# Performance work log

Hardware: AMD Instinct MI355X
Metric: run time of the kernel (lower is better)

## Reference

```python
import jax, jax.numpy as jnp
import numpy as np

N, C, E = 50000, 128, 10
INV3 = float(1.0 / np.sqrt(3.0))
NORM_C = float(1.0 / np.sqrt(C))


def setup_inputs() -> dict:
    key = jax.random.key(0)
    ks = jax.random.split(key, 14)
    node_feats = jax.random.normal(ks[0], (N, 4 * C), jnp.float32)
    elem = jax.random.randint(ks[1], (N,), 0, E)
    node_attrs = jax.nn.one_hot(elem, E, dtype=jnp.float32)
    sc = jax.random.normal(ks[2], (N, 4 * C), jnp.float32)
    tp2_w = jax.random.normal(ks[3], (4, C), jnp.float32)
    tp3_w = jax.random.normal(ks[4], (8, C), jnp.float32)
    coef0_w0 = jax.random.normal(ks[5], (E, C, C), jnp.float32)
    coef0_w1 = jax.random.normal(ks[6], (E, C, C), jnp.float32)
    coef1_w0 = jax.random.normal(ks[7], (E, 2 * C, C), jnp.float32)
    coef1_w1 = jax.random.normal(ks[8], (E, 2 * C, C), jnp.float32)
    coef2_w0 = jax.random.normal(ks[9], (E, 4 * C, C), jnp.float32)
    coef2_w1 = jax.random.normal(ks[10], (E, 4 * C, C), jnp.float32)
    lin_w0 = jax.random.normal(ks[11], (C, C), jnp.float32)
    lin_w1 = jax.random.normal(ks[12], (C, C), jnp.float32)
    return dict(node_feats=node_feats, node_attrs=node_attrs, sc=sc,
                tp2_w=tp2_w, tp3_w=tp3_w,
                coef0_w0=coef0_w0, coef0_w1=coef0_w1,
                coef1_w0=coef1_w0, coef1_w1=coef1_w1,
                coef2_w0=coef2_w0, coef2_w1=coef2_w1,
                lin_w0=lin_w0, lin_w1=lin_w1)


def acc_elem_linear(x0, x1, attrs, W0, W1):
    # per-element linear combine: one-hot attrs select element-specific weights
    norm = 1.0 / np.sqrt(x0.shape[1])
    o0 = jnp.zeros((attrs.shape[0], W0.shape[2]), x0.dtype)
    o1 = jnp.zeros((attrs.shape[0], W1.shape[2], 3), x1.dtype)
    for e in range(W0.shape[0]):  # small fixed element count
        a = attrs[:, e]
        o0 = o0 + a[:, None] * (x0 @ W0[e])
        o1 = o1 + a[:, None, None] * jnp.einsum('ncm,cd->ndm', x1, W1[e])
    return o0 * norm, o1 * norm


def reference(node_feats, node_attrs, sc, tp2_w, tp3_w,
              coef0_w0, coef0_w1, coef1_w0, coef1_w1,
              coef2_w0, coef2_w1, lin_w0, lin_w1):
    n = node_feats.shape[0]
    s = node_feats[:, :C]                      # [N,C]    0e
    v = node_feats[:, C:].reshape(n, C, 3)     # [N,C,3]  1o

    # nu=2: channelwise (uuu) CG tensor product, paths filtered to {0e,1o}
    m0a = tp2_w[0] * s * s                                # 0e x 0e -> 0e
    m1a = tp2_w[1][:, None] * s[:, :, None] * v * INV3    # 0e x 1o -> 1o
    m1b = tp2_w[2][:, None] * v * s[:, :, None] * INV3    # 1o x 0e -> 1o
    m0b = tp2_w[3] * jnp.sum(v * v, axis=-1) * INV3       # 1o x 1o -> 0e

    # nu=3: mid (A0=m0a 0e, A1=m1a 1o, A2=m1b 1o, A3=m0b 0e) x node_feats
    q0 = jnp.concatenate([
        tp3_w[0] * m0a * s,
        tp3_w[3] * jnp.sum(m1a * v, -1) * INV3,
        tp3_w[5] * jnp.sum(m1b * v, -1) * INV3,
        tp3_w[6] * m0b * s], axis=1)                      # [N,4C]
    q1 = jnp.concatenate([
        tp3_w[1][:, None] * m0a[:, :, None] * v * INV3,
        tp3_w[2][:, None] * m1a * s[:, :, None] * INV3,
        tp3_w[4][:, None] * m1b * s[:, :, None] * INV3,
        tp3_w[7][:, None] * m0b[:, :, None] * v * INV3], axis=1)  # [N,4C,3]

    f0, f1 = acc_elem_linear(s, v, node_attrs, coef0_w0, coef0_w1)
    g0, g1 = acc_elem_linear(jnp.concatenate([m0a, m0b], 1),
                             jnp.concatenate([m1a, m1b], 1),
                             node_attrs, coef1_w0, coef1_w1)
    h0, h1 = acc_elem_linear(q0, q1, node_attrs, coef2_w0, coef2_w1)
    o0 = f0 + g0 + h0
    o1 = f1 + g1 + h1

    o0 = (o0 @ lin_w0) * NORM_C
    o1 = jnp.einsum('ncm,cd->ndm', o1, lin_w1) * NORM_C
    out = jnp.concatenate([o0, o1.reshape(n, -1)], axis=1) + sc
    return out
```

## Files before the change

kernel.cpp:

```cpp
#include <hip/hip_runtime.h>

typedef unsigned short u16;
typedef __attribute__((ext_vector_type(8))) short short8;
typedef __attribute__((ext_vector_type(4))) float f32x4;

#define N_NODES 50000
#define C_ 128
#define E_ 10
#define NT_ 16
#define NBLK_MAIN 3200
#define NBLK_S 196
#define K0_ 640
#define K1_ 512

#define WF0_BYTES (E_ * 8 * 20 * 512 * 2)
#define WF1_BYTES (E_ * 8 * 16 * 512 * 2)
#define CNT_OFF    (WF0_BYTES + WF1_BYTES)
#define BLKCNT_OFF (CNT_OFF + 64)
#define BASE_OFF   (BLKCNT_OFF + 8192)
#define LIST_OFF   (BASE_OFF + 8192)

__device__ __forceinline__ u16 f2bf(float f){ union{unsigned u; float f;} v; v.f = f; unsigned u = v.u; u += 0x7FFFu + ((u>>16)&1u); return (u16)(u>>16); }
__device__ __forceinline__ unsigned cvtpk(float a, float b){
    unsigned r;
    asm("v_cvt_pk_bf16_f32 %0, %1, %2" : "=v"(r) : "v"(a), "v"(b));
    return r;
}

__global__ __launch_bounds__(256) void prep_weights_kernel(
    const float* __restrict__ tp2, const float* __restrict__ tp3,
    const float* __restrict__ c00, const float* __restrict__ c10, const float* __restrict__ c20,
    const float* __restrict__ c01, const float* __restrict__ c11, const float* __restrict__ c21,
    const float* __restrict__ lin0, const float* __restrict__ lin1,
    u16* __restrict__ WF0, u16* __restrict__ WF1)
{
    const int b = blockIdx.x;
    const int e = b / 9, kb = b % 9;
    const int which = (kb >= 5) ? 1 : 0;
    const int seg = which ? kb - 5 : kb;
    const float* __restrict__ lin = which ? lin1 : lin0;

    __shared__ u16 R[128 * 136];
    __shared__ u16 LT[128 * 132];

    const int tid = threadIdx.x;
    const float NC = 0.08838834764831845f;

    for (int t = tid; t < 128 * 32; t += 256) {
        const int jj = t >> 5, c4 = (t & 31) << 2;
        const float4 v = *(const float4*)(lin + jj * 128 + c4);
        LT[(c4 + 0) * 132 + jj] = f2bf(v.x * NC);
        LT[(c4 + 1) * 132 + jj] = f2bf(v.y * NC);
        LT[(c4 + 2) * 132 + jj] = f2bf(v.z * NC);
        LT[(c4 + 3) * 132 + jj] = f2bf(v.w * NC);
    }

    {
        const int c = tid >> 1, jh = (tid & 1) * 64;
        const float i128 = 0.08838834764831845f;
        const float i256 = 0.0625f;
        const float i512 = 0.04419417382415922f;
        const float I3   = 0.5773502691896258f;
        const float I9   = I3 * I3;
        const float t2_0 = tp2[0*C_+c], t2_1 = tp2[1*C_+c], t2_2 = tp2[2*C_+c], t2_3 = tp2[3*C_+c];
        const float t3_0 = tp3[0*C_+c], t3_1 = tp3[1*C_+c], t3_2 = tp3[2*C_+c];
        const float t3_3 = tp3[3*C_+c], t3_4 = tp3[4*C_+c], t3_5 = tp3[5*C_+c];
        const float t3_6 = tp3[6*C_+c], t3_7 = tp3[7*C_+c];

        const float* P0; const float* P1 = nullptr; const float* P2 = nullptr;
        float a0 = 0.f, a1 = 0.f, a2 = 0.f;
        if (!which) {
            const float* C0 = c00 + (size_t)e * C_   * C_;
            const float* C1 = c10 + (size_t)e * 2*C_ * C_;
            const float* C2 = c20 + (size_t)e * 4*C_ * C_;
            switch (seg) {
            case 0: P0 = C0 + c*C_;          a0 = i128; break;
            case 1: P0 = C1 + c*C_;          a0 = t2_0 * i256; break;
            case 2: P0 = C1 + (C_+c)*C_;     a0 = t2_3 * I3 * i256; break;
            case 3: P0 = C2 + c*C_;          a0 = t3_0 * t2_0 * i512; break;
            default:
                P0 = C2 + (C_+c)*C_;         a0 = t3_3 * t2_1 * I9 * i512;
                P1 = C2 + (2*C_+c)*C_;       a1 = t3_5 * t2_2 * I9 * i512;
                P2 = C2 + (3*C_+c)*C_;       a2 = t3_6 * t2_3 * I3 * i512; break;
            }
        } else {
            const float* C0 = c01 + (size_t)e * C_   * C_;
            const float* C1 = c11 + (size_t)e * 2*C_ * C_;
            const float* C2 = c21 + (size_t)e * 4*C_ * C_;
            switch (seg) {
            case 0: P0 = C0 + c*C_;          a0 = i128; break;
            case 1: P0 = C1 + c*C_;          a0 = t2_1 * I3 * i256;
                    P1 = C1 + (C_+c)*C_;     a1 = t2_2 * I3 * i256; break;
            case 2: P0 = C2 + c*C_;          a0 = t3_1 * t2_0 * I3 * i512;
                    P1 = C2 + (C_+c)*C_;     a1 = t3_2 * t2_1 * I9 * i512;
                    P2 = C2 + (2*C_+c)*C_;   a2 = t3_4 * t2_2 * I9 * i512; break;
            default: P0 = C2 + (3*C_+c)*C_;  a0 = t3_7 * t2_3 * I9 * i512; break;
            }
        }
        for (int j4 = 0; j4 < 64; j4 += 4) {
            const int jj = jh + j4;
            const float4 v = *(const float4*)(P0 + jj);
            float r0 = a0*v.x, r1 = a0*v.y, r2 = a0*v.z, r3 = a0*v.w;
            if (P1) {
                const float4 u = *(const float4*)(P1 + jj);
                r0 += a1*u.x; r1 += a1*u.y; r2 += a1*u.z; r3 += a1*u.w;
            }
            if (P2) {
                const float4 u = *(const float4*)(P2 + jj);
                r0 += a2*u.x; r1 += a2*u.y; r2 += a2*u.z; r3 += a2*u.w;
            }
            ushort4 st; st.x = f2bf(r0); st.y = f2bf(r1); st.z = f2bf(r2); st.w = f2bf(r3);
            *(ushort4*)&R[c * 136 + jj] = st;
        }
    }
    __syncthreads();

    const int wv = tid >> 6, l = tid & 63;
    const int lcol = l & 15, gD = l >> 4;
    f32x4 acc[2][8];
#pragma unroll
    for (int s = 0; s < 2; ++s)
#pragma unroll
        for (int t = 0; t < 8; ++t) acc[s][t] = (f32x4){0.f, 0.f, 0.f, 0.f};

#pragma unroll
    for (int ks2 = 0; ks2 < 4; ++ks2) {
        const int jj0 = ks2 * 32 + gD * 4;
        short8 bf[8];
#pragma unroll
        for (int t = 0; t < 8; ++t) {
            const int colB = t * 16 + lcol;
            union { unsigned long long q[2]; short8 v; } u;
            u.q[0] = *(const unsigned long long*)&LT[colB * 132 + jj0];
            u.q[1] = *(const unsigned long long*)&LT[colB * 132 + jj0 + 16];
            bf[t] = u.v;
        }
#pragma unroll
        for (int s = 0; s < 2; ++s) {
            const int krow = (wv + s * 4) * 16 + lcol;
            union { unsigned long long q[2]; short8 v; } ua;
            ua.q[0] = *(const unsigned long long*)&R[krow * 136 + jj0];
            ua.q[1] = *(const unsigned long long*)&R[krow * 136 + jj0 + 16];
#pragma unroll
            for (int t = 0; t < 8; ++t)
                acc[s][t] = __builtin_amdgcn_mfma_f32_16x16x32_bf16(ua.v, bf[t], acc[s][t], 0, 0, 0);
        }
    }

#pragma unroll
    for (int s = 0; s < 2; ++s) {
#pragma unroll
        for (int r = 0; r < 4; ++r) {
            const int k = (wv + s * 4) * 16 + 4 * gD + r;
            const int ks = k >> 5, r2 = k & 31;
            const int eh = r2 >> 4, g2 = (r2 >> 2) & 3, el = r2 & 3;
            const int elem = eh * 4 + el;
            const int lanef = lcol + 16 * g2;
            const int slot = seg * 4 + ks;
#pragma unroll
            for (int t = 0; t < 8; ++t) {
                const u16 wvl = f2bf(acc[s][t][r]);
                if (!which) WF0[(((size_t)(e*8 + t))*20 + slot)*512 + lanef*8 + elem] = wvl;
                else        WF1[(((size_t)(e*8 + t))*16 + slot)*512 + lanef*8 + elem] = wvl;
            }
        }
    }
}

__global__ void count_kernel(const float* __restrict__ attrs, int* __restrict__ blkcnt) {
    __shared__ int lcnt[E_];
    const int blk = blockIdx.x, tid = threadIdx.x;
    if (tid < E_) lcnt[tid] = 0;
    __syncthreads();
    const int n = blk * 256 + tid;
    if (n < N_NODES) {
        const float* a = attrs + (size_t)n * E_;
        int e = 0;
#pragma unroll
        for (int i = 0; i < E_; ++i) if (a[i] > 0.5f) e = i;
        atomicAdd(&lcnt[e], 1);
    }
    __syncthreads();
    if (tid < E_) blkcnt[tid * 200 + blk] = lcnt[tid];
}

__global__ void scan_kernel(const int* __restrict__ blkcnt, int* __restrict__ base,
                            int* __restrict__ cnt) {
    const int e = threadIdx.x;
    if (e < E_) {
        int acc = 0;
        for (int b = 0; b < NBLK_S; ++b) { base[e * 200 + b] = acc; acc += blkcnt[e * 200 + b]; }
        cnt[e] = acc;
    }
}

__global__ void scatter_kernel(const float* __restrict__ attrs, const int* __restrict__ base,
                               int* __restrict__ lists) {
    __shared__ int wcnt[4][E_];
    __shared__ int wbase[4][E_];
    const int blk = blockIdx.x, tid = threadIdx.x;
    const int wv = tid >> 6, lane = tid & 63;
    const int n = blk * 256 + tid;
    int e = -1;
    if (n < N_NODES) {
        e = 0;
        const float* a = attrs + (size_t)n * E_;
#pragma unroll
        for (int i = 0; i < E_; ++i) if (a[i] > 0.5f) e = i;
    }
    int rank = 0;
#pragma unroll
    for (int v = 0; v < E_; ++v) {
        const unsigned long long m = __ballot(e == v);
        if (e == v) rank = __popcll(m & ((1ull << lane) - 1ull));
        if (lane == 0) wcnt[wv][v] = __popcll(m);
    }
    __syncthreads();
    if (tid < E_) {
        int acc = 0;
#pragma unroll
        for (int w2 = 0; w2 < 4; ++w2) { wbase[w2][tid] = acc; acc += wcnt[w2][tid]; }
    }
    __syncthreads();
    if (n < N_NODES) lists[e * N_NODES + base[e * 200 + blk] + wbase[wv][e] + rank] = n;
}

__global__ __launch_bounds__(256, 3) void main_kernel(
    const float* __restrict__ feats, const float* __restrict__ sc,
    const int* __restrict__ cnt, const int* __restrict__ lists,
    const u16* __restrict__ WF0, const u16* __restrict__ WF1,
    float* __restrict__ out)
{
    __shared__ __align__(16) u16 A2[2][24 * 512];

    const int tid = threadIdx.x;
    const int bxr = blockIdx.x;
    const int bx = (bxr & 7) * (NBLK_MAIN / 8) + (bxr >> 3);

    int e = -1, tile = 0, accT = 0;
#pragma unroll
    for (int i = 0; i < E_; ++i) {
        const int ci = cnt[i];
        const int t = (ci + NT_ - 1) >> 4;
        if (e < 0 && bx < accT + t) { e = i; tile = bx - accT; }
        accT += t;
    }
    if (e < 0) return;
    const int nvalid = min(NT_, cnt[e] - tile * NT_);

    const int node = tid >> 4;
    const int cg   = tid & 15;
    const int n = (node < nvalid) ? lists[e*N_NODES + tile*NT_ + node] : -1;

    float4 s0 = make_float4(0.f,0.f,0.f,0.f), s1 = s0;
    float4 v4[6];
#pragma unroll
    for (int k = 0; k < 6; ++k) v4[k] = s0;
    if (n >= 0) {
        const float* f = feats + (size_t)n * 512;
        s0 = *(const float4*)(f + cg*8);
        s1 = *(const float4*)(f + cg*8 + 4);
#pragma unroll
        for (int k = 0; k < 6; ++k) v4[k] = *(const float4*)(f + 128 + cg*24 + 4*k);
    }
    float S[8]  = {s0.x,s0.y,s0.z,s0.w, s1.x,s1.y,s1.z,s1.w};
    float V[24] = {v4[0].x,v4[0].y,v4[0].z,v4[0].w, v4[1].x,v4[1].y,v4[1].z,v4[1].w,
                   v4[2].x,v4[2].y,v4[2].z,v4[2].w, v4[3].x,v4[3].y,v4[3].z,v4[3].w,
                   v4[4].x,v4[4].y,v4[4].z,v4[4].w, v4[5].x,v4[5].y,v4[5].z,v4[5].w};
    float S2[8], VV[8];
#pragma unroll
    for (int i = 0; i < 8; ++i) {
        S2[i] = S[i]*S[i];
        VV[i] = V[3*i]*V[3*i] + V[3*i+1]*V[3*i+1] + V[3*i+2]*V[3*i+2];
    }

    const int ksl   = cg >> 2;
    const int eh    = (cg >> 1) & 1;
    const int gb    = (cg & 1) * 2;
    const int lp0   = (node + 16*gb)        ^ (ksl << 1);
    const int lp1   = (node + 16*(gb + 1))  ^ (ksl << 1);
    const int off0  = lp0*8 + 4*eh;
    const int off1  = lp1*8 + 4*eh;

#define WSLOT(BUF, SLOT, V0,V1,V2,V3,V4,V5,V6,V7) do { \
        uint2 w0_, w1_; \
        w0_.x = cvtpk((V0),(V1)); w0_.y = cvtpk((V2),(V3)); \
        w1_.x = cvtpk((V4),(V5)); w1_.y = cvtpk((V6),(V7)); \
        *(uint2*)&A2[BUF][(SLOT)*512 + off0] = w0_; \
        *(uint2*)&A2[BUF][(SLOT)*512 + off1] = w1_; \
    } while (0)

    WSLOT(0, 0*4 + ksl, S[0],S[1],S[2],S[3],S[4],S[5],S[6],S[7]);
    WSLOT(0, 1*4 + ksl, S2[0],S2[1],S2[2],S2[3],S2[4],S2[5],S2[6],S2[7]);
    WSLOT(0, 2*4 + ksl, VV[0],VV[1],VV[2],VV[3],VV[4],VV[5],VV[6],VV[7]);
    WSLOT(0, 3*4 + ksl, S2[0]*S[0],S2[1]*S[1],S2[2]*S[2],S2[3]*S[3],
                        S2[4]*S[4],S2[5]*S[5],S2[6]*S[6],S2[7]*S[7]);
    WSLOT(0, 4*4 + ksl, S[0]*VV[0],S[1]*VV[1],S[2]*VV[2],S[3]*VV[3],
                        S[4]*VV[4],S[5]*VV[5],S[6]*VV[6],S[7]*VV[7]);
    __syncthreads();

    const int w4 = tid >> 6, l = tid & 63;
    const int lcol = l & 15, g = l >> 4;
    const int col0 = (2*w4)*16 + lcol;
    const int col1 = col0 + 16;
    const u16* WB0a = WF0 + ((size_t)(e*8 + 2*w4))     * (20*512) + l*8;
    const u16* WB0b = WB0a + 20*512;
    const u16* WB1a = WF1 + ((size_t)(e*8 + 2*w4))     * (16*512) + l*8;
    const u16* WB1b = WB1a + 16*512;

    f32x4 accS0 = {0.f,0.f,0.f,0.f}, accS1 = accS0;
    f32x4 accV[3][2];
#pragma unroll
    for (int m = 0; m < 3; ++m) { accV[m][0] = accS0; accV[m][1] = accS0; }

#pragma unroll
    for (int m = 0; m < 3; ++m) {
        WSLOT(1, m*4 + ksl,     V[0*3+m],V[1*3+m],V[2*3+m],V[3*3+m],
                                V[4*3+m],V[5*3+m],V[6*3+m],V[7*3+m]);
        WSLOT(1, (3+m)*4 + ksl, S[0]*V[0*3+m],S[1]*V[1*3+m],S[2]*V[2*3+m],S[3]*V[3*3+m],
                                S[4]*V[4*3+m],S[5]*V[5*3+m],S[6]*V[6*3+m],S[7]*V[7*3+m]);
    }
#pragma unroll
    for (int ks2 = 0; ks2 < 4; ++ks2) {
        const int lp8 = (l ^ (ks2 << 1)) * 8;
#pragma unroll
        for (int p = 0; p < 5; ++p) {
            const short8 a  = *(const short8*)&A2[0][(p*4 + ks2)*512 + lp8];
            const short8 b0 = *(const short8*)(WB0a + (p*4 + ks2)*512);
            const short8 b1 = *(const short8*)(WB0b + (p*4 + ks2)*512);
            accS0 = __builtin_amdgcn_mfma_f32_16x16x32_bf16(a, b0, accS0, 0, 0, 0);
            accS1 = __builtin_amdgcn_mfma_f32_16x16x32_bf16(a, b1, accS1, 0, 0, 0);
        }
    }
    __syncthreads();

#pragma unroll
    for (int m = 0; m < 3; ++m) {
        WSLOT(0, m*4 + ksl,     S2[0]*V[0*3+m],S2[1]*V[1*3+m],S2[2]*V[2*3+m],S2[3]*V[3*3+m],
                                S2[4]*V[4*3+m],S2[5]*V[5*3+m],S2[6]*V[6*3+m],S2[7]*V[7*3+m]);
        WSLOT(0, (3+m)*4 + ksl, VV[0]*V[0*3+m],VV[1]*V[1*3+m],VV[2]*V[2*3+m],VV[3]*V[3*3+m],
                                VV[4]*V[4*3+m],VV[5]*V[5*3+m],VV[6]*V[6*3+m],VV[7]*V[7*3+m]);
    }
    float4 scR[8];
#pragma unroll
    for (int j = 0; j < 8; ++j) scR[j] = make_float4(0.f,0.f,0.f,0.f);
    if (n >= 0) {
        const float* sp = sc + (size_t)n * 512 + cg * 4;
#pragma unroll
        for (int j = 0; j < 8; ++j) scR[j] = *(const float4*)(sp + 64*j);
    }
#pragma unroll
    for (int ks2 = 0; ks2 < 4; ++ks2) {
        const int lp8 = (l ^ (ks2 << 1)) * 8;
#pragma unroll
        for (int q = 0; q < 2; ++q) {
            const short8 b0 = *(const short8*)(WB1a + (q*4 + ks2)*512);
            const short8 b1 = *(const short8*)(WB1b + (q*4 + ks2)*512);
#pragma unroll
            for (int m = 0; m < 3; ++m) {
                const short8 a = *(const short8*)&A2[1][((q*3 + m)*4 + ks2)*512 + lp8];
                accV[m][0] = __builtin_amdgcn_mfma_f32_16x16x32_bf16(a, b0, accV[m][0], 0, 0, 0);
                accV[m][1] = __builtin_amdgcn_mfma_f32_16x16x32_bf16(a, b1, accV[m][1], 0, 0, 0);
            }
        }
    }
    __syncthreads();

#pragma unroll
    for (int ks2 = 0; ks2 < 4; ++ks2) {
        const int lp8 = (l ^ (ks2 << 1)) * 8;
#pragma unroll
        for (int q = 0; q < 2; ++q) {
            const short8 b0 = *(const short8*)(WB1a + ((2+q)*4 + ks2)*512);
            const short8 b1 = *(const short8*)(WB1b + ((2+q)*4 + ks2)*512);
#pragma unroll
            for (int m = 0; m < 3; ++m) {
                const short8 a = *(const short8*)&A2[0][((q*3 + m)*4 + ks2)*512 + lp8];
                accV[m][0] = __builtin_amdgcn_mfma_f32_16x16x32_bf16(a, b0, accV[m][0], 0, 0, 0);
                accV[m][1] = __builtin_amdgcn_mfma_f32_16x16x32_bf16(a, b1, accV[m][1], 0, 0, 0);
            }
        }
    }
    __syncthreads();

    float* OutB = (float*)&A2[0][0];
#pragma unroll
    for (int r = 0; r < 4; ++r) {
        const int nd = 4*g + r;
        OutB[nd*516 + col0] = accS0[r];
        OutB[nd*516 + col1] = accS1[r];
#pragma unroll
        for (int m = 0; m < 3; ++m) {
            OutB[nd*516 + 128 + 3*col0 + m] = accV[m][0][r];
            OutB[nd*516 + 128 + 3*col1 + m] = accV[m][1][r];
        }
    }
    __syncthreads();

    if (n >= 0) {
        const size_t gb2 = (size_t)n * 512 + cg * 4;
#pragma unroll
        for (int j = 0; j < 8; ++j) {
            const float4 vres = *(const float4*)&OutB[node*516 + cg*4 + 64*j];
            float4 o;
            o.x = vres.x + scR[j].x; o.y = vres.y + scR[j].y;
            o.z = vres.z + scR[j].z; o.w = vres.w + scR[j].w;
            *(float4*)(out + gb2 + 64*j) = o;
        }
    }
#undef WSLOT
}

extern "C" void kernel_launch(void* const* d_in, const int* in_sizes, int n_in,
                              void* d_out, int out_size, void* d_ws, size_t ws_size,
                              hipStream_t stream) {
    const float* feats = (const float*)d_in[0];
    const float* attrs = (const float*)d_in[1];
    const float* sc    = (const float*)d_in[2];
    const float* tp2   = (const float*)d_in[3];
    const float* tp3   = (const float*)d_in[4];
    const float* c00   = (const float*)d_in[5];
    const float* c01   = (const float*)d_in[6];
    const float* c10   = (const float*)d_in[7];
    const float* c11   = (const float*)d_in[8];
    const float* c20   = (const float*)d_in[9];
    const float* c21   = (const float*)d_in[10];
    const float* lin0  = (const float*)d_in[11];
    const float* lin1  = (const float*)d_in[12];
    float* out = (float*)d_out;

    char* ws = (char*)d_ws;
    u16* WF0    = (u16*)(ws);
    u16* WF1    = (u16*)(ws + WF0_BYTES);
    int* cnt    = (int*)(ws + CNT_OFF);
    int* blkcnt = (int*)(ws + BLKCNT_OFF);
    int* base   = (int*)(ws + BASE_OFF);
    int* lists  = (int*)(ws + LIST_OFF);

    hipLaunchKernelGGL(prep_weights_kernel, dim3(E_*9), dim3(256), 0, stream,
                       tp2, tp3, c00, c10, c20, c01, c11, c21, lin0, lin1, WF0, WF1);
    hipLaunchKernelGGL(count_kernel, dim3(NBLK_S), dim3(256), 0, stream, attrs, blkcnt);
    hipLaunchKernelGGL(scan_kernel, dim3(1), dim3(64), 0, stream, blkcnt, base, cnt);
    hipLaunchKernelGGL(scatter_kernel, dim3(NBLK_S), dim3(256), 0, stream, attrs, base, lists);
    hipLaunchKernelGGL(main_kernel, dim3(NBLK_MAIN), dim3(256), 0, stream,
                       feats, sc, cnt, lists, WF0, WF1, out);
}
```

Measured before the change: 119.5 us.

## Process 32 nodes per block with 8 waves sharing weight fragments

Doubles the node tile to 32 and the block to 512 threads. Each of the 8 waves now owns one 16-column output slice and applies the same weight fragment to two 16-node halves, so the weight loads from global memory are shared across more nodes. The double-buffered A staging is replaced by a single larger buffer with extra barriers, which serializes staging and MFMA phases. The output is written back in two passes, and the sc load moves into the epilogue, so more synchronization is traded for less weight traffic.

```diff
diff --git a/kernel.cpp b/kernel.cpp
--- a/kernel.cpp
+++ b/kernel.cpp
@@ -7,8 +7,8 @@
 #define N_NODES 50000
 #define C_ 128
 #define E_ 10
-#define NT_ 16
-#define NBLK_MAIN 3200
+#define NT_ 32
+#define NBLK_MAIN 1600
 #define NBLK_S 196
 #define K0_ 640
 #define K1_ 512
@@ -225,13 +225,13 @@
     if (n < N_NODES) lists[e * N_NODES + base[e * 200 + blk] + wbase[wv][e] + rank] = n;
 }
 
-__global__ __launch_bounds__(256, 3) void main_kernel(
+__global__ __launch_bounds__(512, 4) void main_kernel(
     const float* __restrict__ feats, const float* __restrict__ sc,
     const int* __restrict__ cnt, const int* __restrict__ lists,
     const u16* __restrict__ WF0, const u16* __restrict__ WF1,
     float* __restrict__ out)
 {
-    __shared__ __align__(16) u16 A2[2][24 * 512];
+    __shared__ __align__(16) u16 A[24 * 1024];
 
     const int tid = threadIdx.x;
     const int bxr = blockIdx.x;
@@ -241,7 +241,7 @@
 #pragma unroll
     for (int i = 0; i < E_; ++i) {
         const int ci = cnt[i];
-        const int t = (ci + NT_ - 1) >> 4;
+        const int t = (ci + NT_ - 1) >> 5;
         if (e < 0 && bx < accT + t) { e = i; tile = bx - accT; }
         accT += t;
     }
@@ -250,6 +250,8 @@
 
     const int node = tid >> 4;
     const int cg   = tid & 15;
+    const int h    = node >> 4;
+    const int nodeL = node & 15;
     const int n = (node < nvalid) ? lists[e*N_NODES + tile*NT_ + node] : -1;
 
     float4 s0 = make_float4(0.f,0.f,0.f,0.f), s1 = s0;
@@ -274,138 +276,149 @@
         VV[i] = V[3*i]*V[3*i] + V[3*i+1]*V[3*i+1] + V[3*i+2]*V[3*i+2];
     }
 
-    const int ksl   = cg >> 2;
-    const int eh    = (cg >> 1) & 1;
-    const int gb    = (cg & 1) * 2;
-    const int lp0   = (node + 16*gb)        ^ (ksl << 1);
-    const int lp1   = (node + 16*(gb + 1))  ^ (ksl << 1);
-    const int off0  = lp0*8 + 4*eh;
-    const int off1  = lp1*8 + 4*eh;
-
-#define WSLOT(BUF, SLOT, V0,V1,V2,V3,V4,V5,V6,V7) do { \
+    const int ksl = cg >> 2;
+    const int eh  = (cg >> 1) & 1;
+    const int gb  = (cg & 1) * 2;
+    const int off0 = h*512 + (((nodeL + 16*gb)     ^ (ksl << 1)))*8 + 4*eh;
+    const int off1 = h*512 + (((nodeL + 16*(gb+1)) ^ (ksl << 1)))*8 + 4*eh;
+
+#define WSLOT(SLOT, V0,V1,V2,V3,V4,V5,V6,V7) do { \
         uint2 w0_, w1_; \
         w0_.x = cvtpk((V0),(V1)); w0_.y = cvtpk((V2),(V3)); \
         w1_.x = cvtpk((V4),(V5)); w1_.y = cvtpk((V6),(V7)); \
-        *(uint2*)&A2[BUF][(SLOT)*512 + off0] = w0_; \
-        *(uint2*)&A2[BUF][(SLOT)*512 + off1] = w1_; \
+        *(uint2*)&A[(SLOT)*1024 + off0] = w0_; \
+        *(uint2*)&A[(SLOT)*1024 + off1] = w1_; \
     } while (0)
 
-    WSLOT(0, 0*4 + ksl, S[0],S[1],S[2],S[3],S[4],S[5],S[6],S[7]);
-    WSLOT(0, 1*4 + ksl, S2[0],S2[1],S2[2],S2[3],S2[4],S2[5],S2[6],S2[7]);
-    WSLOT(0, 2*4 + ksl, VV[0],VV[1],VV[2],VV[3],VV[4],VV[5],VV[6],VV[7]);
-    WSLOT(0, 3*4 + ksl, S2[0]*S[0],S2[1]*S[1],S2[2]*S[2],S2[3]*S[3],
-                        S2[4]*S[4],S2[5]*S[5],S2[6]*S[6],S2[7]*S[7]);
-    WSLOT(0, 4*4 + ksl, S[0]*VV[0],S[1]*VV[1],S[2]*VV[2],S[3]*VV[3],
-                        S[4]*VV[4],S[5]*VV[5],S[6]*VV[6],S[7]*VV[7]);
-    __syncthreads();
-
-    const int w4 = tid >> 6, l = tid & 63;
+    const int w = tid >> 6, l = tid & 63;
     const int lcol = l & 15, g = l >> 4;
-    const int col0 = (2*w4)*16 + lcol;
-    const int col1 = col0 + 16;
-    const u16* WB0a = WF0 + ((size_t)(e*8 + 2*w4))     * (20*512) + l*8;
-    const u16* WB0b = WB0a + 20*512;
-    const u16* WB1a = WF1 + ((size_t)(e*8 + 2*w4))     * (16*512) + l*8;
-    const u16* WB1b = WB1a + 16*512;
+    const int col = w*16 + lcol;
+    const u16* WB0 = WF0 + ((size_t)(e*8 + w)) * (20*512) + l*8;
+    const u16* WB1 = WF1 + ((size_t)(e*8 + w)) * (16*512) + l*8;
 
     f32x4 accS0 = {0.f,0.f,0.f,0.f}, accS1 = accS0;
-    f32x4 accV[3][2];
-#pragma unroll
-    for (int m = 0; m < 3; ++m) { accV[m][0] = accS0; accV[m][1] = accS0; }
+    f32x4 aV[3][2];
+#pragma unroll
+    for (int m = 0; m < 3; ++m) { aV[m][0] = accS0; aV[m][1] = accS0; }
+
+    WSLOT(0*4 + ksl, S[0],S[1],S[2],S[3],S[4],S[5],S[6],S[7]);
+    WSLOT(1*4 + ksl, S2[0],S2[1],S2[2],S2[3],S2[4],S2[5],S2[6],S2[7]);
+    WSLOT(2*4 + ksl, VV[0],VV[1],VV[2],VV[3],VV[4],VV[5],VV[6],VV[7]);
+    WSLOT(3*4 + ksl, S2[0]*S[0],S2[1]*S[1],S2[2]*S[2],S2[3]*S[3],
+                     S2[4]*S[4],S2[5]*S[5],S2[6]*S[6],S2[7]*S[7]);
+    WSLOT(4*4 + ksl, S[0]*VV[0],S[1]*VV[1],S[2]*VV[2],S[3]*VV[3],
+                     S[4]*VV[4],S[5]*VV[5],S[6]*VV[6],S[7]*VV[7]);
+    __syncthreads();
+
+#pragma unroll
+    for (int ks2 = 0; ks2 < 4; ++ks2) {
+        short8 bS[5];
+#pragma unroll
+        for (int p = 0; p < 5; ++p) bS[p] = *(const short8*)(WB0 + (p*4 + ks2)*512);
+        const int lp8 = (l ^ (ks2 << 1)) * 8;
+#pragma unroll
+        for (int p = 0; p < 5; ++p) {
+            const short8 a0 = *(const short8*)&A[(p*4 + ks2)*1024 + lp8];
+            const short8 a1 = *(const short8*)&A[(p*4 + ks2)*1024 + 512 + lp8];
+            accS0 = __builtin_amdgcn_mfma_f32_16x16x32_bf16(a0, bS[p], accS0, 0, 0, 0);
+            accS1 = __builtin_amdgcn_mfma_f32_16x16x32_bf16(a1, bS[p], accS1, 0, 0, 0);
+        }
+    }
+    __syncthreads();
 
 #pragma unroll
     for (int m = 0; m < 3; ++m) {
-        WSLOT(1, m*4 + ksl,     V[0*3+m],V[1*3+m],V[2*3+m],V[3*3+m],
-                                V[4*3+m],V[5*3+m],V[6*3+m],V[7*3+m]);
-        WSLOT(1, (3+m)*4 + ksl, S[0]*V[0*3+m],S[1]*V[1*3+m],S[2]*V[2*3+m],S[3]*V[3*3+m],
-                                S[4]*V[4*3+m],S[5]*V[5*3+m],S[6]*V[6*3+m],S[7]*V[7*3+m]);
-    }
+        WSLOT(m*4 + ksl,     V[0+m],V[3+m],V[6+m],V[9+m],V[12+m],V[15+m],V[18+m],V[21+m]);
+        WSLOT((3+m)*4 + ksl, S[0]*V[0+m],S[1]*V[3+m],S[2]*V[6+m],S[3]*V[9+m],
+                             S[4]*V[12+m],S[5]*V[15+m],S[6]*V[18+m],S[7]*V[21+m]);
+    }
+    __syncthreads();
+
 #pragma unroll
     for (int ks2 = 0; ks2 < 4; ++ks2) {
+        const short8 b0 = *(const short8*)(WB1 + (0*4 + ks2)*512);
+        const short8 b1 = *(const short8*)(WB1 + (1*4 + ks2)*512);
         const int lp8 = (l ^ (ks2 << 1)) * 8;
 #pragma unroll
-        for (int p = 0; p < 5; ++p) {
-            const short8 a  = *(const short8*)&A2[0][(p*4 + ks2)*512 + lp8];
-            const short8 b0 = *(const short8*)(WB0a + (p*4 + ks2)*512);
-            const short8 b1 = *(const short8*)(WB0b + (p*4 + ks2)*512);
-            accS0 = __builtin_amdgcn_mfma_f32_16x16x32_bf16(a, b0, accS0, 0, 0, 0);
-            accS1 = __builtin_amdgcn_mfma_f32_16x16x32_bf16(a, b1, accS1, 0, 0, 0);
+        for (int q = 0; q < 2; ++q) {
+            const short8 bb = q ? b1 : b0;
+#pragma unroll
+            for (int m = 0; m < 3; ++m) {
+                const short8 a0 = *(const short8*)&A[((q*3 + m)*4 + ks2)*1024 + lp8];
+                const short8 a1 = *(const short8*)&A[((q*3 + m)*4 + ks2)*1024 + 512 + lp8];
+                aV[m][0] = __builtin_amdgcn_mfma_f32_16x16x32_bf16(a0, bb, aV[m][0], 0, 0, 0);
+                aV[m][1] = __builtin_amdgcn_mfma_f32_16x16x32_bf16(a1, bb, aV[m][1], 0, 0, 0);
+            }
         }
     }
     __syncthreads();
 
 #pragma unroll
     for (int m = 0; m < 3; ++m) {
-        WSLOT(0, m*4 + ksl,     S2[0]*V[0*3+m],S2[1]*V[1*3+m],S2[2]*V[2*3+m],S2[3]*V[3*3+m],
-                                S2[4]*V[4*3+m],S2[5]*V[5*3+m],S2[6]*V[6*3+m],S2[7]*V[7*3+m]);
-        WSLOT(0, (3+m)*4 + ksl, VV[0]*V[0*3+m],VV[1]*V[1*3+m],VV[2]*V[2*3+m],VV[3]*V[3*3+m],
-                                VV[4]*V[4*3+m],VV[5]*V[5*3+m],VV[6]*V[6*3+m],VV[7]*V[7*3+m]);
-    }
-    float4 scR[8];
-#pragma unroll
-    for (int j = 0; j < 8; ++j) scR[j] = make_float4(0.f,0.f,0.f,0.f);
-    if (n >= 0) {
-        const float* sp = sc + (size_t)n * 512 + cg * 4;
-#pragma unroll
-        for (int j = 0; j < 8; ++j) scR[j] = *(const float4*)(sp + 64*j);
-    }
+        WSLOT(m*4 + ksl,     S2[0]*V[0+m],S2[1]*V[3+m],S2[2]*V[6+m],S2[3]*V[9+m],
+                             S2[4]*V[12+m],S2[5]*V[15+m],S2[6]*V[18+m],S2[7]*V[21+m]);
+        WSLOT((3+m)*4 + ksl, VV[0]*V[0+m],VV[1]*V[3+m],VV[2]*V[6+m],VV[3]*V[9+m],
+                             VV[4]*V[12+m],VV[5]*V[15+m],VV[6]*V[18+m],VV[7]*V[21+m]);
+    }
+    __syncthreads();
+
 #pragma unroll
     for (int ks2 = 0; ks2 < 4; ++ks2) {
+        const short8 b2 = *(const short8*)(WB1 + (2*4 + ks2)*512);
+        const short8 b3 = *(const short8*)(WB1 + (3*4 + ks2)*512);
         const int lp8 = (l ^ (ks2 << 1)) * 8;
 #pragma unroll
         for (int q = 0; q < 2; ++q) {
-            const short8 b0 = *(const short8*)(WB1a + (q*4 + ks2)*512);
-            const short8 b1 = *(const short8*)(WB1b + (q*4 + ks2)*512);
+            const short8 bb = q ? b3 : b2;
 #pragma unroll
             for (int m = 0; m < 3; ++m) {
-                const short8 a = *(const short8*)&A2[1][((q*3 + m)*4 + ks2)*512 + lp8];
-                accV[m][0] = __builtin_amdgcn_mfma_f32_16x16x32_bf16(a, b0, accV[m][0], 0, 0, 0);
-                accV[m][1] = __builtin_amdgcn_mfma_f32_16x16x32_bf16(a, b1, accV[m][1], 0, 0, 0);
-            }
-        }
-    }
-    __syncthreads();
-
-#pragma unroll
-    for (int ks2 = 0; ks2 < 4; ++ks2) {
-        const int lp8 = (l ^ (ks2 << 1)) * 8;
-#pragma unroll
-        for (int q = 0; q < 2; ++q) {
-            const short8 b0 = *(const short8*)(WB1a + ((2+q)*4 + ks2)*512);
-            const short8 b1 = *(const short8*)(WB1b + ((2+q)*4 + ks2)*512);
-#pragma unroll
-            for (int m = 0; m < 3; ++m) {
-                const short8 a = *(const short8*)&A2[0][((q*3 + m)*4 + ks2)*512 + lp8];
-                accV[m][0] = __builtin_amdgcn_mfma_f32_16x16x32_bf16(a, b0, accV[m][0], 0, 0, 0);
-                accV[m][1] = __builtin_amdgcn_mfma_f32_16x16x32_bf16(a, b1, accV[m][1], 0, 0, 0);
-            }
-        }
-    }
-    __syncthreads();
-
-    float* OutB = (float*)&A2[0][0];
+                const short8 a0 = *(const short8*)&A[((q*3 + m)*4 + ks2)*1024 + lp8];
+                const short8 a1 = *(const short8*)&A[((q*3 + m)*4 + ks2)*1024 + 512 + lp8];
+                aV[m][0] = __builtin_amdgcn_mfma_f32_16x16x32_bf16(a0, bb, aV[m][0], 0, 0, 0);
+                aV[m][1] = __builtin_amdgcn_mfma_f32_16x16x32_bf16(a1, bb, aV[m][1], 0, 0, 0);
+            }
+        }
+    }
+    __syncthreads();
+
+    float* OutB = (float*)&A[0];
+
 #pragma unroll
     for (int r = 0; r < 4; ++r) {
         const int nd = 4*g + r;
-        OutB[nd*516 + col0] = accS0[r];
-        OutB[nd*516 + col1] = accS1[r];
-#pragma unroll
-        for (int m = 0; m < 3; ++m) {
-            OutB[nd*516 + 128 + 3*col0 + m] = accV[m][0][r];
-            OutB[nd*516 + 128 + 3*col1 + m] = accV[m][1][r];
-        }
-    }
-    __syncthreads();
-
-    if (n >= 0) {
+        OutB[nd*516 + col] = accS0[r];
+#pragma unroll
+        for (int m = 0; m < 3; ++m) OutB[nd*516 + 128 + 3*col + m] = aV[m][0][r];
+    }
+    __syncthreads();
+    if (h == 0 && n >= 0) {
         const size_t gb2 = (size_t)n * 512 + cg * 4;
+        const float* sp = sc + gb2;
 #pragma unroll
         for (int j = 0; j < 8; ++j) {
-            const float4 vres = *(const float4*)&OutB[node*516 + cg*4 + 64*j];
-            float4 o;
-            o.x = vres.x + scR[j].x; o.y = vres.y + scR[j].y;
-            o.z = vres.z + scR[j].z; o.w = vres.w + scR[j].w;
-            *(float4*)(out + gb2 + 64*j) = o;
+            const f32x4 vres = *(const f32x4*)&OutB[nodeL*516 + cg*4 + 64*j];
+            const f32x4 s4   = *(const f32x4*)(sp + 64*j);
+            *(f32x4*)(out + gb2 + 64*j) = vres + s4;
+        }
+    }
+    __syncthreads();
+
+#pragma unroll
+    for (int r = 0; r < 4; ++r) {
+        const int nd = 4*g + r;
+        OutB[nd*516 + col] = accS1[r];
+#pragma unroll
+        for (int m = 0; m < 3; ++m) OutB[nd*516 + 128 + 3*col + m] = aV[m][1][r];
+    }
+    __syncthreads();
+    if (h == 1 && n >= 0) {
+        const size_t gb2 = (size_t)n * 512 + cg * 4;
+        const float* sp = sc + gb2;
+#pragma unroll
+        for (int j = 0; j < 8; ++j) {
+            const f32x4 vres = *(const f32x4*)&OutB[nodeL*516 + cg*4 + 64*j];
+            const f32x4 s4   = *(const f32x4*)(sp + 64*j);
+            *(f32x4*)(out + gb2 + 64*j) = vres + s4;
         }
     }
 #undef WSLOT
@@ -442,6 +455,6 @@
     hipLaunchKernelGGL(count_kernel, dim3(NBLK_S), dim3(256), 0, stream, attrs, blkcnt);
     hipLaunchKernelGGL(scan_kernel, dim3(1), dim3(64), 0, stream, blkcnt, base, cnt);
     hipLaunchKernelGGL(scatter_kernel, dim3(NBLK_S), dim3(256), 0, stream, attrs, base, lists);
-    hipLaunchKernelGGL(main_kernel, dim3(NBLK_MAIN), dim3(256), 0, stream,
+    hipLaunchKernelGGL(main_kernel, dim3(NBLK_MAIN), dim3(512), 0, stream,
                        feats, sc, cnt, lists, WF0, WF1, out);
 }
```

Result: faster. 112.4 us, median of 3 (-5.9%).
